# Optimization experiments

Measured on AMD Instinct MI355X. Metric: run time of the kernel, lower is better.

Reference implementation:

```python
import jax, jax.numpy as jnp
import numpy as np

ROI_SIZE = 7
SPATIAL_SCALE = 1.0 / 16.0
CHUNK = 16  # rois processed per lax.map step to bound the masked-max intermediate


def roi_pool(x, indices_and_rois):
    """Caffe-style RoI max pooling. x: [N,C,H,W]; indices_and_rois: [R,5]=(idx,x1,y1,x2,y2)."""
    N, C, H, W = x.shape
    P = ROI_SIZE
    hi = jnp.arange(H, dtype=x.dtype)
    wi = jnp.arange(W, dtype=x.dtype)
    p = jnp.arange(P, dtype=x.dtype)

    def pool_one(r5):
        idx = r5[0].astype(jnp.int32)
        xmin, ymin, xmax, ymax = r5[1], r5[2], r5[3], r5[4]
        sw = jnp.round(xmin * SPATIAL_SCALE)
        sh = jnp.round(ymin * SPATIAL_SCALE)
        ew = jnp.round(xmax * SPATIAL_SCALE)
        eh = jnp.round(ymax * SPATIAL_SCALE)
        bw = jnp.maximum(ew - sw + 1.0, 1.0) / P  # bin width in feature cells
        bh = jnp.maximum(eh - sh + 1.0, 1.0) / P
        wstart = jnp.clip(jnp.floor(p * bw) + sw, 0.0, float(W))
        wend = jnp.clip(jnp.ceil((p + 1.0) * bw) + sw, 0.0, float(W))
        hstart = jnp.clip(jnp.floor(p * bh) + sh, 0.0, float(H))
        hend = jnp.clip(jnp.ceil((p + 1.0) * bh) + sh, 0.0, float(H))
        colmask = (wi[None, :] >= wstart[:, None]) & (wi[None, :] < wend[:, None])  # [P,W]
        rowmask = (hi[None, :] >= hstart[:, None]) & (hi[None, :] < hend[:, None])  # [P,H]
        img = x[idx]  # [C,H,W] gather of the roi's image
        neg = jnp.asarray(-jnp.inf, x.dtype)
        # max over columns within each column-bin, then over rows within each row-bin
        m1 = jnp.max(jnp.where(colmask[None, None, :, :], img[:, :, None, :], neg), axis=-1)  # [C,H,P]
        m2 = jnp.max(jnp.where(rowmask[None, :, :, None], m1[:, None, :, :], neg), axis=2)  # [C,P,P]
        return jnp.where(jnp.isfinite(m2), m2, jnp.zeros((), x.dtype))  # empty bins -> 0

    R = indices_and_rois.shape[0]
    chunks = indices_and_rois.reshape(R // CHUNK, CHUNK, 5)
    pooled = jax.lax.map(jax.vmap(pool_one), chunks)  # [R//CHUNK, CHUNK, C, P, P]
    return pooled.reshape(R, C, P, P)


def setup_inputs() -> dict:
    key = jax.random.key(0)
    ks = jax.random.split(key, 8)
    N, C, H, W = 4, 512, 50, 50  # 800x800 image, VGG16 stride 16
    R, n_class = 512, 21
    x = jax.random.normal(ks[0], (N, C, H, W), jnp.float32)
    yx1 = jax.random.uniform(ks[1], (R, 2), jnp.float32, 0.0, 700.0)
    wh = jax.random.uniform(ks[2], (R, 2), jnp.float32, 32.0, 128.0)
    rois = jnp.concatenate([yx1, jnp.minimum(yx1 + wh, 799.0)], axis=1)  # (y1,x1,y2,x2)
    roi_indices = jax.random.randint(ks[3], (R,), 0, N)
    din = C * ROI_SIZE * ROI_SIZE
    W1 = jax.random.normal(ks[4], (din, 4096), jnp.float32) * 0.01
    b1 = jnp.zeros((4096,), jnp.float32)
    W2 = jax.random.normal(ks[5], (4096, 4096), jnp.float32) * 0.01
    b2 = jnp.zeros((4096,), jnp.float32)
    Wc = jax.random.normal(ks[6], (4096, n_class * 4), jnp.float32) * 0.001
    bc = jnp.zeros((n_class * 4,), jnp.float32)
    Ws = jax.random.normal(ks[7], (4096, n_class), jnp.float32) * 0.01
    bs = jnp.zeros((n_class,), jnp.float32)
    return {"x": x, "rois": rois, "roi_indices": roi_indices, "W1": W1, "b1": b1,
            "W2": W2, "b2": b2, "Wc": Wc, "bc": bc, "Ws": Ws, "bs": bs}


def reference(x, rois, roi_indices, W1, b1, W2, b2, Wc, bc, Ws, bs):
    # concat index + boxes, then reorder (idx,y1,x1,y2,x2) -> (idx,x1,y1,x2,y2)
    ir = jnp.concatenate([roi_indices[:, None].astype(jnp.float32), rois], axis=1)
    ir = ir[:, jnp.array([0, 2, 1, 4, 3])]
    pool = roi_pool(x, ir)  # [R, C, 7, 7]
    flat = pool.reshape(pool.shape[0], -1)  # [R, 25088]
    fc6 = jax.nn.relu(flat @ W1 + b1)
    fc7 = jax.nn.relu(fc6 @ W2 + b2)
    roi_cls_locs = fc7 @ Wc + bc  # [R, n_class*4]
    roi_scores = fc7 @ Ws + bs  # [R, n_class]
    return (roi_cls_locs, roi_scores)
```

## Files before the change

kernel.cpp:

```cpp
#include <hip/hip_runtime.h>
#include <math.h>

typedef __attribute__((ext_vector_type(8))) short short8;
typedef __attribute__((ext_vector_type(4))) short s16x4;
typedef __attribute__((ext_vector_type(4))) float f32x4;
typedef __attribute__((ext_vector_type(4))) unsigned u32x4;

#define R_ROIS 512
#define CCH 512
#define HH 50
#define WW 50
#define PPOOL 7
#define KDIM (CCH * PPOOL * PPOOL)
#define NH 4096
#define ZSPLIT 8
#define NHEAD 105

__device__ __forceinline__ short f2bf(float f) {
  unsigned u = __builtin_bit_cast(unsigned, f);
  u += 0x7FFFu + ((u >> 16) & 1u);
  return (short)(u >> 16);
}
__device__ __forceinline__ float bf2f(short s) {
  unsigned u = ((unsigned)(unsigned short)s) << 16;
  return __builtin_bit_cast(float, u);
}
__device__ __forceinline__ unsigned cvtpk(float lo, float hi) {
  unsigned r;
  asm("v_cvt_pk_bf16_f32 %0, %1, %2" : "=v"(r) : "v"(lo), "v"(hi));
  return r;
}

__global__ __launch_bounds__(256) void roi_pool_kernel(
    const float* __restrict__ x, const float* __restrict__ rois,
    const int* __restrict__ ridx, short* __restrict__ A) {
  __shared__ int hs[PPOOL], he[PPOOL], wss[PPOOL], wee[PPOOL];
  __shared__ int sidx;
  const int r = blockIdx.x;
  if (threadIdx.x == 0) {
    float ymin = rois[r * 4 + 0], xmin = rois[r * 4 + 1];
    float ymax = rois[r * 4 + 2], xmax = rois[r * 4 + 3];
    float sw = rintf(xmin * 0.0625f);
    float sh = rintf(ymin * 0.0625f);
    float ew = rintf(xmax * 0.0625f);
    float eh = rintf(ymax * 0.0625f);
    float bw = fmaxf(ew - sw + 1.0f, 1.0f) * (1.0f / 7.0f);
    float bh = fmaxf(eh - sh + 1.0f, 1.0f) * (1.0f / 7.0f);
    for (int p = 0; p < PPOOL; ++p) {
      wss[p] = (int)fminf(fmaxf(floorf(p * bw) + sw, 0.0f), 50.0f);
      wee[p] = (int)fminf(fmaxf(ceilf((p + 1) * bw) + sw, 0.0f), 50.0f);
      hs[p]  = (int)fminf(fmaxf(floorf(p * bh) + sh, 0.0f), 50.0f);
      he[p]  = (int)fminf(fmaxf(ceilf((p + 1) * bh) + sh, 0.0f), 50.0f);
    }
    sidx = ridx[r];
  }
  __syncthreads();
  const float* xb = x + (size_t)sidx * CCH * HH * WW;
  const int obeg = blockIdx.y * (KDIM / 8), oend = obeg + KDIM / 8;
  for (int o = obeg + threadIdx.x; o < oend; o += 256) {
    int c = o / 49;
    int pq = o - c * 49;
    int ph = pq / 7, pw = pq - ph * 7;
    const float* xc = xb + (size_t)c * (HH * WW);
    int h0 = hs[ph], h1 = he[ph], w0 = wss[pw], w1 = wee[pw];
    float mv = -INFINITY;
    for (int h = h0; h < h1; ++h) {
      const float* xr = xc + h * WW;
      for (int w = w0; w < w1; ++w) mv = fmaxf(mv, xr[w]);
    }
    A[(size_t)r * KDIM + o] = f2bf((h1 > h0 && w1 > w0) ? mv : 0.0f);
  }
}

__global__ __launch_bounds__(512, 2) void gemm_splitk_kernel(
    const short* __restrict__ A, const float* __restrict__ B,
    float* __restrict__ part, int M, int N, int K, int Ks, int nblk) {
  __shared__ __align__(16) char As[2][256 * 64];
  __shared__ __align__(16) char Bs[2][256 * 64];
  const int bid = blockIdx.x;
  const int vid = (bid & 7) * (nblk >> 3) + (bid >> 3);
  const int mb = vid & 1;
  const int nb = (vid >> 1) & 15;
  const int zb = vid >> 5;
  const int m0 = mb * 256, n0 = nb * 256;
  const int kbeg = zb * Ks, kend = kbeg + Ks;
  const int t = threadIdx.x;
  const int lane = t & 63, wid = t >> 6;
  const int wm = wid >> 2, wn = wid & 3;
  const int lr = lane & 15, kc = lane >> 4;
  const int ar = t >> 1, ah = t & 1;
  const int bn = t & 255, bko = t >> 8;

  const short* aptrA = A + (size_t)(m0 + ar) * K + ah * 16;
  const float* bbase = B + n0 + bn;

  const int awz0 = (ar * 64 + ah * 32) ^ ((ar & 7) << 4);
  const int awz1 = awz0 ^ 16;
  const int bwz0 = (bn * 64 + bko * 32) ^ ((bn & 7) << 4);
  const int bwz1 = bwz0 ^ 16;
  const int aoff = (wm * 8192 + lr * 64 + kc * 16) ^ ((lr & 7) << 4);
  const int boff = (wn * 4096 + lr * 64 + kc * 16) ^ ((lr & 7) << 4);

  f32x4 acc[8][4] = {};
  short8 a_r0, a_r1;
  float br[16];

  auto LOADT = [&](int k0) {
    a_r0 = *(const short8*)(aptrA + k0);
    a_r1 = *(const short8*)(aptrA + k0 + 8);
    const float* bp = bbase + (size_t)(k0 + bko * 16) * N;
    #pragma unroll
    for (int j = 0; j < 16; ++j) br[j] = bp[(size_t)j * N];
  };
  auto WRITET = [&](int buf) {
    *(short8*)(As[buf] + awz0) = a_r0;
    *(short8*)(As[buf] + awz1) = a_r1;
    u32x4 w0, w1;
    w0[0] = cvtpk(br[0], br[1]);   w0[1] = cvtpk(br[2], br[3]);
    w0[2] = cvtpk(br[4], br[5]);   w0[3] = cvtpk(br[6], br[7]);
    w1[0] = cvtpk(br[8], br[9]);   w1[1] = cvtpk(br[10], br[11]);
    w1[2] = cvtpk(br[12], br[13]); w1[3] = cvtpk(br[14], br[15]);
    *(u32x4*)(Bs[buf] + bwz0) = w0;
    *(u32x4*)(Bs[buf] + bwz1) = w1;
  };
  auto COMPUTE = [&](int buf) {
    short8 b[4];
    #pragma unroll
    for (int n = 0; n < 4; ++n)
      b[n] = *(const short8*)(Bs[buf] + boff + n * 1024);
    #pragma unroll
    for (int m = 0; m < 8; ++m) {
      short8 a = *(const short8*)(As[buf] + aoff + m * 1024);
      #pragma unroll
      for (int n = 0; n < 4; ++n)
        acc[m][n] = __builtin_amdgcn_mfma_f32_16x16x32_bf16(a, b[n], acc[m][n], 0, 0, 0);
    }
  };

  LOADT(kbeg);
  WRITET(0);
  __syncthreads();

  int cur = 0;
  for (int k0 = kbeg + 32; k0 <= kend; k0 += 32) {
    bool more = (k0 < kend);
    if (more) LOADT(k0);
    COMPUTE(cur);
    if (more) {
      WRITET(cur ^ 1);
      __syncthreads();
      cur ^= 1;
    }
  }

  float* pz = part + (size_t)zb * M * N;
  #pragma unroll
  for (int m = 0; m < 8; ++m) {
    #pragma unroll
    for (int n = 0; n < 4; ++n) {
      int col = n0 + wn * 64 + n * 16 + lr;
      #pragma unroll
      for (int j = 0; j < 4; ++j) {
        int row = m0 + wm * 128 + m * 16 + kc * 4 + j;
        pz[(size_t)row * N + col] = acc[m][n][j];
      }
    }
  }
}

__global__ __launch_bounds__(256) void reduce_relu_kernel(
    const float* __restrict__ part, const float* __restrict__ bias,
    short* __restrict__ out, int MN, int N) {
  int i = (blockIdx.x * 256 + threadIdx.x) * 4;
  if (i >= MN) return;
  const float4 b = *(const float4*)(bias + (i & (N - 1)));
  float4 s = *(const float4*)(part + i);
  #pragma unroll
  for (int z = 1; z < ZSPLIT; ++z) {
    float4 p = *(const float4*)(part + (size_t)z * MN + i);
    s.x += p.x; s.y += p.y; s.z += p.z; s.w += p.w;
  }
  s16x4 o;
  o.x = f2bf(fmaxf(s.x + b.x, 0.0f));
  o.y = f2bf(fmaxf(s.y + b.y, 0.0f));
  o.z = f2bf(fmaxf(s.z + b.z, 0.0f));
  o.w = f2bf(fmaxf(s.w + b.w, 0.0f));
  *(s16x4*)(out + i) = o;
}

__global__ __launch_bounds__(256) void pack_head_w_kernel(
    const float* __restrict__ Wc, const float* __restrict__ Wsv,
    short* __restrict__ Wt) {
  const int n = blockIdx.x;
  for (int k = threadIdx.x; k < NH; k += 256) {
    float v = 0.0f;
    if (n < 84) v = Wc[(size_t)k * 84 + n];
    else if (n < NHEAD) v = Wsv[(size_t)k * 21 + (n - 84)];
    Wt[(size_t)n * NH + k] = f2bf(v);
  }
}

__global__ __launch_bounds__(256, 2) void gemm_head_kernel(
    const short* __restrict__ A, const short* __restrict__ Bt,
    float* __restrict__ part2) {
  __shared__ __align__(16) char As[2][128 * 64];
  __shared__ __align__(16) char Bs[2][128 * 64];
  const int m0 = blockIdx.x * 128;
  const int zb = blockIdx.y;
  const int kbeg = zb * (NH / ZSPLIT), kend = kbeg + NH / ZSPLIT;
  const int t = threadIdx.x;
  const int lane = t & 63, wid = t >> 6;
  const int wm = wid >> 1, wn = wid & 1;
  const int lr = lane & 15, kc = lane >> 4;
  const int sr = t >> 2, seg = t & 3;

  const short* aptr0 = A + (size_t)(m0 + sr) * NH + seg * 8;
  const short* aptr1 = aptr0 + (size_t)64 * NH;
  const short* bptr0 = Bt + (size_t)sr * NH + seg * 8;
  const short* bptr1 = bptr0 + (size_t)64 * NH;

  const int wz0 = (sr * 64 + seg * 16) ^ ((sr & 7) << 4);
  const int wz1 = wz0 + 4096;
  const int aoff = (wm * 4096 + lr * 64 + kc * 16) ^ ((lr & 7) << 4);
  const int boff = (wn * 4096 + lr * 64 + kc * 16) ^ ((lr & 7) << 4);

  f32x4 acc[4][4] = {};
  short8 a_r0, a_r1, b_r0, b_r1;

  auto LOADT = [&](int k0) {
    a_r0 = *(const short8*)(aptr0 + k0);
    a_r1 = *(const short8*)(aptr1 + k0);
    b_r0 = *(const short8*)(bptr0 + k0);
    b_r1 = *(const short8*)(bptr1 + k0);
  };
  auto WRITET = [&](int buf) {
    *(short8*)(As[buf] + wz0) = a_r0;
    *(short8*)(As[buf] + wz1) = a_r1;
    *(short8*)(Bs[buf] + wz0) = b_r0;
    *(short8*)(Bs[buf] + wz1) = b_r1;
  };
  auto COMPUTE = [&](int buf) {
    short8 a[4], b[4];
    #pragma unroll
    for (int m = 0; m < 4; ++m)
      a[m] = *(const short8*)(As[buf] + aoff + m * 1024);
    #pragma unroll
    for (int n = 0; n < 4; ++n)
      b[n] = *(const short8*)(Bs[buf] + boff + n * 1024);
    #pragma unroll
    for (int m = 0; m < 4; ++m)
      #pragma unroll
      for (int n = 0; n < 4; ++n)
        acc[m][n] = __builtin_amdgcn_mfma_f32_16x16x32_bf16(a[m], b[n], acc[m][n], 0, 0, 0);
  };

  LOADT(kbeg);
  WRITET(0);
  __syncthreads();

  int cur = 0;
  for (int k0 = kbeg + 32; k0 <= kend; k0 += 32) {
    bool more = (k0 < kend);
    if (more) LOADT(k0);
    COMPUTE(cur);
    if (more) {
      WRITET(cur ^ 1);
      __syncthreads();
      cur ^= 1;
    }
  }

  float* pz = part2 + (size_t)zb * R_ROIS * 128;
  #pragma unroll
  for (int m = 0; m < 4; ++m) {
    #pragma unroll
    for (int n = 0; n < 4; ++n) {
      int col = wn * 64 + n * 16 + lr;
      #pragma unroll
      for (int j = 0; j < 4; ++j) {
        int row = m0 + wm * 64 + m * 16 + kc * 4 + j;
        pz[(size_t)row * 128 + col] = acc[m][n][j];
      }
    }
  }
}

__global__ __launch_bounds__(128) void reduce_head_kernel(
    const float* __restrict__ part2, const float* __restrict__ bc,
    const float* __restrict__ bs, float* __restrict__ out) {
  const int r = blockIdx.x, c = threadIdx.x;
  if (c >= NHEAD) return;
  float s = 0.0f;
  #pragma unroll
  for (int z = 0; z < ZSPLIT; ++z)
    s += part2[(size_t)z * R_ROIS * 128 + (size_t)r * 128 + c];
  if (c < 84)
    out[(size_t)r * 84 + c] = s + bc[c];
  else
    out[(size_t)R_ROIS * 84 + (size_t)r * 21 + (c - 84)] = s + bs[c - 84];
}

extern "C" void kernel_launch(void* const* d_in, const int* in_sizes, int n_in,
                              void* d_out, int out_size, void* d_ws, size_t ws_size,
                              hipStream_t stream) {
  const float* x    = (const float*)d_in[0];
  const float* rois = (const float*)d_in[1];
  const int*   ridx = (const int*)d_in[2];
  const float* W1   = (const float*)d_in[3];
  const float* b1   = (const float*)d_in[4];
  const float* W2   = (const float*)d_in[5];
  const float* b2   = (const float*)d_in[6];
  const float* Wc   = (const float*)d_in[7];
  const float* bc   = (const float*)d_in[8];
  const float* Wsv  = (const float*)d_in[9];
  const float* bs   = (const float*)d_in[10];

  const int MN = R_ROIS * NH;
  short* A     = (short*)d_ws;
  short* fc6   = A + (size_t)R_ROIS * KDIM;
  short* fc7   = fc6 + (size_t)MN;
  float* part  = (float*)(fc7 + (size_t)MN);
  float* part2 = part + (size_t)ZSPLIT * MN;
  short* Wt    = (short*)(part2 + (size_t)ZSPLIT * R_ROIS * 128);

  roi_pool_kernel<<<dim3(R_ROIS, 8), 256, 0, stream>>>(x, rois, ridx, A);
  pack_head_w_kernel<<<128, 256, 0, stream>>>(Wc, Wsv, Wt);

  gemm_splitk_kernel<<<256, 512, 0, stream>>>(A, W1, part, R_ROIS, NH, KDIM,
                                              KDIM / ZSPLIT, 256);
  reduce_relu_kernel<<<MN / 4 / 256, 256, 0, stream>>>(part, b1, fc6, MN, NH);

  gemm_splitk_kernel<<<256, 512, 0, stream>>>(fc6, W2, part, R_ROIS, NH, NH,
                                              NH / ZSPLIT, 256);
  reduce_relu_kernel<<<MN / 4 / 256, 256, 0, stream>>>(part, b2, fc7, MN, NH);

  gemm_head_kernel<<<dim3(4, ZSPLIT), 256, 0, stream>>>(fc7, Wt, part2);
  reduce_head_kernel<<<R_ROIS, 128, 0, stream>>>(part2, bc, bs, (float*)d_out);
}
```

Measured before the change: 308.9 us.

## Deepen global-load prefetch to two stages and use barriers without vmcnt drain

The fc6 split-K GEMM main loop is unrolled by two and alternates between two register sets, so global loads for tile k+2 are in flight while tile k+1 is written to LDS and tile k is computed. __syncthreads is replaced by a barrier that waits only on lgkmcnt, so outstanding global loads no longer drain at each barrier. The change aims to hide the latency of the strided fp32 B loads. In exchange it doubles the prefetch register footprint, which risks spills under launch_bounds(512,2). The loop also assumes an even step count, and correctness now depends on the compiler inserting vmcnt waits before the register data is used.

```diff
diff --git a/kernel.cpp b/kernel.cpp
--- a/kernel.cpp
+++ b/kernel.cpp
@@ -15,6 +15,12 @@
 #define NH 4096
 #define ZSPLIT 8
 #define NHEAD 105
+
+#define BARRIER_NO_VMDRAIN()                              \
+  do {                                                    \
+    asm volatile("s_waitcnt lgkmcnt(0)" ::: "memory");    \
+    __builtin_amdgcn_s_barrier();                         \
+  } while (0)
 
 __device__ __forceinline__ short f2bf(float f) {
   unsigned u = __builtin_bit_cast(unsigned, f);
@@ -83,7 +89,8 @@
   const int nb = (vid >> 1) & 15;
   const int zb = vid >> 5;
   const int m0 = mb * 256, n0 = nb * 256;
-  const int kbeg = zb * Ks, kend = kbeg + Ks;
+  const int kbeg = zb * Ks;
+  const int S = Ks >> 5;
   const int t = threadIdx.x;
   const int lane = t & 63, wid = t >> 6;
   const int wm = wid >> 2, wn = wid & 3;
@@ -102,19 +109,19 @@
   const int boff = (wn * 4096 + lr * 64 + kc * 16) ^ ((lr & 7) << 4);
 
   f32x4 acc[8][4] = {};
-  short8 a_r0, a_r1;
-  float br[16];
-
-  auto LOADT = [&](int k0) {
-    a_r0 = *(const short8*)(aptrA + k0);
-    a_r1 = *(const short8*)(aptrA + k0 + 8);
+  short8 aA0, aA1, aB0, aB1;
+  float bA[16], bB[16];
+
+  auto LOADT = [&](int k0, short8& r0, short8& r1, float* br) {
+    r0 = *(const short8*)(aptrA + k0);
+    r1 = *(const short8*)(aptrA + k0 + 8);
     const float* bp = bbase + (size_t)(k0 + bko * 16) * N;
     #pragma unroll
     for (int j = 0; j < 16; ++j) br[j] = bp[(size_t)j * N];
   };
-  auto WRITET = [&](int buf) {
-    *(short8*)(As[buf] + awz0) = a_r0;
-    *(short8*)(As[buf] + awz1) = a_r1;
+  auto WRITET = [&](int buf, const short8& r0, const short8& r1, const float* br) {
+    *(short8*)(As[buf] + awz0) = r0;
+    *(short8*)(As[buf] + awz1) = r1;
     u32x4 w0, w1;
     w0[0] = cvtpk(br[0], br[1]);   w0[1] = cvtpk(br[2], br[3]);
     w0[2] = cvtpk(br[4], br[5]);   w0[3] = cvtpk(br[6], br[7]);
@@ -137,18 +144,23 @@
     }
   };
 
-  LOADT(kbeg);
-  WRITET(0);
-  __syncthreads();
+  LOADT(kbeg, aA0, aA1, bA);
+  WRITET(0, aA0, aA1, bA);
+  LOADT(kbeg + 32, aB0, aB1, bB);
+  BARRIER_NO_VMDRAIN();
 
   int cur = 0;
-  for (int k0 = kbeg + 32; k0 <= kend; k0 += 32) {
-    bool more = (k0 < kend);
-    if (more) LOADT(k0);
+  for (int i = 0; i < S; i += 2) {
+    if (i + 2 < S) LOADT(kbeg + (i + 2) * 32, aA0, aA1, bA);
     COMPUTE(cur);
-    if (more) {
-      WRITET(cur ^ 1);
-      __syncthreads();
+    WRITET(cur ^ 1, aB0, aB1, bB);
+    BARRIER_NO_VMDRAIN();
+    cur ^= 1;
+    if (i + 3 < S) LOADT(kbeg + (i + 3) * 32, aB0, aB1, bB);
+    COMPUTE(cur);
+    if (i + 2 < S) {
+      WRITET(cur ^ 1, aA0, aA1, bA);
+      BARRIER_NO_VMDRAIN();
       cur ^= 1;
     }
   }
@@ -256,7 +268,7 @@
 
   LOADT(kbeg);
   WRITET(0);
-  __syncthreads();
+  BARRIER_NO_VMDRAIN();
 
   int cur = 0;
   for (int k0 = kbeg + 32; k0 <= kend; k0 += 32) {
@@ -265,7 +277,7 @@
     COMPUTE(cur);
     if (more) {
       WRITET(cur ^ 1);
-      __syncthreads();
+      BARRIER_NO_VMDRAIN();
       cur ^= 1;
     }
   }
```

Result: faster. 294.1 us (-4.8%).
